# Optimization experiments

Measured on AMD Instinct MI355X. Metric: run time of the kernel, lower is better.

## Reference

```python
import jax, jax.numpy as jnp
import numpy as np

N, FR, P, B = 8192, 128, 4194304, 64
LH1, LH2 = 128, 64

def _mlp(x, W1, b1, W2, b2, W3, b3):
    h = jnp.tanh(x @ W1 + b1)
    h = jnp.tanh(h @ W2 + b2)
    return h @ W3 + b3  # [N, 1]

def setup_inputs() -> dict:
    key = jax.random.key(0)
    ks = jax.random.split(key, 12)
    r = jax.random.normal(ks[0], (N, FR), jnp.float32)
    xyz = jax.random.uniform(ks[1], (N, 3), jnp.float32) * 60.0  # box so distances >> sigma
    p0 = jax.random.randint(ks[2], (P,), 0, N)
    off = jax.random.randint(ks[3], (P,), 1, N)  # avoid self-pairs (D2=0)
    pairs = jnp.stack([p0, (p0 + off) % N], axis=1).astype(jnp.int32)
    num_pairs = jnp.full((B,), P // B, dtype=jnp.int32)
    def lin(k, fin, fout):
        return (jax.random.normal(k, (fin, fout), jnp.float32) / np.sqrt(fin)).astype(jnp.float32)
    sW1, sW2, sW3 = lin(ks[4], FR, LH1), lin(ks[5], LH1, LH2), lin(ks[6], LH2, 1)
    eW1, eW2, eW3 = lin(ks[7], FR, LH1), lin(ks[8], LH1, LH2), lin(ks[9], LH2, 1)
    z1, z2, z3 = jnp.zeros((LH1,), jnp.float32), jnp.zeros((LH2,), jnp.float32), jnp.zeros((1,), jnp.float32)
    return dict(r=r, xyz=xyz, pairs=pairs, num_pairs=num_pairs,
                sW1=sW1, sb1=z1, sW2=sW2, sb2=z2, sW3=sW3, sb3=z3,
                eW1=eW1, eb1=z1, eW2=eW2, eb2=z2, eW3=eW3, eb3=z3)

def reference(r, xyz, pairs, num_pairs, sW1, sb1, sW2, sb2, sW3, sb3,
              eW1, eb1, eW2, eb2, eW3, eb3):
    # D2 gathered at pairs == squared distance between the two atoms of each pair
    dx = xyz[pairs[:, 1]] - xyz[pairs[:, 0]]          # [P, 3]
    D2 = jnp.sum(dx * dx, axis=1, keepdims=True)       # [P, 1]
    inv_D = D2 ** -0.5
    sigma = 4.0 + 10.0 * _mlp(r, sW1, sb1, sW2, sb2, sW3, sb3) ** 2   # [N, 1]
    epsilon = 0.1 * _mlp(r, eW1, eb1, eW2, eb2, eW3, eb3) ** 2        # [N, 1]
    sigma_mixed = jnp.sqrt(sigma[pairs[:, 0]] * sigma[pairs[:, 1]])    # [P, 1]
    epsilon_mixed = jnp.sqrt(epsilon[pairs[:, 0]] * epsilon[pairs[:, 1]])
    s = sigma_mixed * inv_D
    s6 = s ** 6
    E_pair = 4.0 * epsilon_mixed * (s6 * s6 - s6)       # [P, 1]
    seg = jnp.repeat(jnp.arange(B), num_pairs, total_repeat_length=P)
    E = jax.ops.segment_sum(E_pair, seg, num_segments=B)  # [B, 1]
    return E
```

## Files before the change

### kernel.cpp

```cpp
#include <hip/hip_runtime.h>
#include <hip/hip_fp16.h>

#define NATOM 8192
#define FR    128
#define NSEG  64
#define NPROD 128
#define NBLK  256
#define PT    1024
#define PPT   16
#define SENT  0x5EED1234

typedef _Float16 v8h __attribute__((ext_vector_type(8)));
typedef _Float16 v4h __attribute__((ext_vector_type(4)));
typedef float    v4f __attribute__((ext_vector_type(4)));

__device__ __forceinline__ float fast_tanh(float x)
{
    float t = __expf(2.f * x);
    return 1.f - 2.f * __builtin_amdgcn_rcpf(t + 1.f);
}

__device__ __forceinline__ float pair_e(const float4* atomd, int ia, int ib)
{
    float4 A = atomd[ia], B = atomd[ib];
    float dx = A.x - B.x, dy = A.y - B.y, dz = A.z - B.z;
    float D2 = fmaf(dx, dx, fmaf(dy, dy, dz * dz));
    float inv = __builtin_amdgcn_rcpf(D2);
    float inv3 = inv * inv * inv;
    __half2 ha = __builtin_bit_cast(__half2, A.w);
    __half2 hb = __builtin_bit_cast(__half2, B.w);
    float pp = __low2float(ha) * __low2float(hb);
    float qq = __high2float(ha) * __high2float(hb);
    float s6 = pp * pp * inv3;
    return 4.f * qq * (s6 * s6 - s6);
}

__global__ __launch_bounds__(PT, 4) void k_fused(
    const float* __restrict__ r, const float* __restrict__ xyz,
    const int* __restrict__ pairs, const int* __restrict__ num_pairs,
    const float* __restrict__ w1s, const float* __restrict__ b1s,
    const float* __restrict__ w2s, const float* __restrict__ b2s,
    const float* __restrict__ w3s, const float* __restrict__ b3s,
    const float* __restrict__ w1e, const float* __restrict__ b1e,
    const float* __restrict__ w2e, const float* __restrict__ b2e,
    const float* __restrict__ w3e, const float* __restrict__ b3e,
    float4* __restrict__ atomd, int* __restrict__ flags,
    float* __restrict__ out, int P)
{
    extern __shared__ char ldsraw[];
    const int tid = threadIdx.x;
    const int bid = blockIdx.x;
    const bool prod = (bid < NPROD);

    if (bid == 0 && tid < NSEG) out[tid] = 0.f;

    const int base = (bid * PT + tid) * PPT;
    const bool fast = (base + PPT <= P);
    int pr2[PPT * 2];

    if ((!prod || tid >= 512) && fast) {
        const int4* pp4 = (const int4*)(pairs + (size_t)base * 2);
#pragma unroll
        for (int i = 0; i < PPT / 2; ++i) {
            int4 v = pp4[i];
            pr2[4*i] = v.x; pr2[4*i+1] = v.y; pr2[4*i+2] = v.z; pr2[4*i+3] = v.w;
        }
    }

    {
        _Float16* Wh  = (_Float16*)ldsraw;
        _Float16* Wl  = Wh + 32768;
        _Float16* h1h = Wh;
        _Float16* h1l = Wh + 16384;
        _Float16* W2h = Wh + 32768;
        _Float16* W2l = Wh + 49152;
        float*    mArr = (float*)(ldsraw + 131072);

        const int a0  = bid * 64;
        const int l = tid & 63, wv = tid >> 6;
        const int row16 = l & 15, kgrp = l >> 4;
        const int at = wv & 3, chf = wv >> 2;
        const bool mlp = prod && (tid < 512);

        v8h rh[4], rl[4];
        if (mlp) {
#pragma unroll
            for (int i = 0; i < 8; ++i) {
                int g = i * 512 + tid;
                int c = g & 255, ch = g >> 8;
                const float* wp = (c < 128) ? (w1s + c) : (w1e + (c - 128));
                v8h hh, ll;
#pragma unroll
                for (int j = 0; j < 8; ++j) {
                    float x = wp[(ch * 8 + j) * 128];
                    _Float16 h = (_Float16)x;
                    hh[j] = h;
                    ll[j] = (_Float16)((x - (float)h) * 4096.f);
                }
                int sw = c * 16 + (ch ^ (c & 15));
                *(v8h*)(Wh + sw * 8) = hh;
                *(v8h*)(Wl + sw * 8) = ll;
            }
            const float* rb = r + (size_t)(a0 + at * 16 + row16) * FR + kgrp * 8;
#pragma unroll
            for (int ks = 0; ks < 4; ++ks) {
                float4 x0 = *(const float4*)(rb + ks * 32);
                float4 x1 = *(const float4*)(rb + ks * 32 + 4);
                float xs[8] = {x0.x, x0.y, x0.z, x0.w, x1.x, x1.y, x1.z, x1.w};
#pragma unroll
                for (int j = 0; j < 8; ++j) {
                    _Float16 h = (_Float16)xs[j];
                    rh[ks][j] = h;
                    rl[ks][j] = (_Float16)((xs[j] - (float)h) * 4096.f);
                }
            }
        }
        __syncthreads();

        v4h hpack[8], lpack[8];
        if (mlp) {
#pragma unroll
            for (int ct = 0; ct < 8; ++ct) {
                int crow = chf * 128 + ct * 16 + row16;
                v4f a = {0.f, 0.f, 0.f, 0.f}, cr = {0.f, 0.f, 0.f, 0.f};
                int rbo = crow * 128, sw = crow & 15;
#pragma unroll
                for (int ks = 0; ks < 4; ++ks) {
                    int off = rbo + (((ks * 4 + kgrp) ^ sw) * 8);
                    v8h wh = *(const v8h*)(Wh + off);
                    v8h wl = *(const v8h*)(Wl + off);
                    a  = __builtin_amdgcn_mfma_f32_16x16x32_f16(wh, rh[ks], a,  0, 0, 0);
                    cr = __builtin_amdgcn_mfma_f32_16x16x32_f16(wh, rl[ks], cr, 0, 0, 0);
                    cr = __builtin_amdgcn_mfma_f32_16x16x32_f16(wl, rh[ks], cr, 0, 0, 0);
                }
                int colb = chf * 128 + ct * 16 + kgrp * 4;
                const float* bp = (colb < 128) ? (b1s + colb) : (b1e + (colb - 128));
                float4 bv = *(const float4*)bp;
                float bvx[4] = {bv.x, bv.y, bv.z, bv.w};
#pragma unroll
                for (int j = 0; j < 4; ++j) {
                    float v = fast_tanh(a[j] + cr[j] * 2.44140625e-4f + bvx[j]);
                    _Float16 h = (_Float16)v;
                    hpack[ct][j] = h;
                    lpack[ct][j] = (_Float16)((v - (float)h) * 4096.f);
                }
            }
        }
        __syncthreads();

        if (mlp) {
            int arow = at * 16 + row16;
#pragma unroll
            for (int ct = 0; ct < 8; ++ct) {
                int colb = chf * 128 + ct * 16 + kgrp * 4;
                int chs = (colb >> 3) ^ row16;
                int off = arow * 256 + chs * 8 + (colb & 7);
                *(v4h*)(h1h + off) = hpack[ct];
                *(v4h*)(h1l + off) = lpack[ct];
            }
#pragma unroll
            for (int i = 0; i < 4; ++i) {
                int g = i * 512 + tid;
                int c = g & 127, ch = g >> 7;
                const float* wp = (c < 64) ? (w2s + c) : (w2e + (c - 64));
                v8h hh, ll;
#pragma unroll
                for (int j = 0; j < 8; ++j) {
                    float x = wp[(ch * 8 + j) * 64];
                    _Float16 h = (_Float16)x;
                    hh[j] = h;
                    ll[j] = (_Float16)((x - (float)h) * 4096.f);
                }
                int sw = c * 16 + (ch ^ (c & 15));
                *(v8h*)(W2h + sw * 8) = hh;
                *(v8h*)(W2l + sw * 8) = ll;
            }
        }
        __syncthreads();

        if (mlp) {
            const int arow = at * 16 + row16;
            v8h bh[4], bl[4];
#pragma unroll
            for (int ks = 0; ks < 4; ++ks) {
                int chunk = chf * 16 + ks * 4 + kgrp;
                int off = arow * 256 + ((chunk ^ row16) * 8);
                bh[ks] = *(const v8h*)(h1h + off);
                bl[ks] = *(const v8h*)(h1l + off);
            }
            float ps = 0.f;
#pragma unroll
            for (int ct2 = 0; ct2 < 4; ++ct2) {
                int c2 = chf * 64 + ct2 * 16 + row16;
                v4f a = {0.f, 0.f, 0.f, 0.f}, cr = {0.f, 0.f, 0.f, 0.f};
                int rbo = c2 * 128, sw = c2 & 15;
#pragma unroll
                for (int ks = 0; ks < 4; ++ks) {
                    int off = rbo + (((ks * 4 + kgrp) ^ sw) * 8);
                    v8h wh = *(const v8h*)(W2h + off);
                    v8h wl = *(const v8h*)(W2l + off);
                    a  = __builtin_amdgcn_mfma_f32_16x16x32_f16(wh, bh[ks], a,  0, 0, 0);
                    cr = __builtin_amdgcn_mfma_f32_16x16x32_f16(wh, bl[ks], cr, 0, 0, 0);
                    cr = __builtin_amdgcn_mfma_f32_16x16x32_f16(wl, bh[ks], cr, 0, 0, 0);
                }
                int cb = ct2 * 16 + kgrp * 4;
                float4 b2v = *(const float4*)((chf ? b2e : b2s) + cb);
                float4 w3v = *(const float4*)((chf ? w3e : w3s) + cb);
                float b2x[4] = {b2v.x, b2v.y, b2v.z, b2v.w};
                float w3x[4] = {w3v.x, w3v.y, w3v.z, w3v.w};
#pragma unroll
                for (int j = 0; j < 4; ++j) {
                    float h2 = fast_tanh(a[j] + cr[j] * 2.44140625e-4f + b2x[j]);
                    ps = fmaf(h2, w3x[j], ps);
                }
            }
            ps += __shfl_xor(ps, 16);
            ps += __shfl_xor(ps, 32);
            if (l < 16) mArr[chf * 64 + at * 16 + l] = ps + (chf ? b3e[0] : b3s[0]);
        }
        __syncthreads();

        if (prod && tid < 64) {
            int atom = a0 + tid;
            float ms = mArr[tid], me = mArr[64 + tid];
            float sg = fmaf(10.f * ms, ms, 4.f);
            float p  = sg * sqrtf(sg);
            float q  = 0.31622776601683794f * fabsf(me);
            __half2 pq = __halves2half2(__float2half(p), __float2half(q));
            atomd[atom] = make_float4(xyz[3 * atom], xyz[3 * atom + 1],
                                      xyz[3 * atom + 2], __builtin_bit_cast(float, pq));
        }
        __syncthreads();
        if (prod && tid == 0) {
            __threadfence();
            __hip_atomic_store(&flags[bid], SENT, __ATOMIC_RELEASE, __HIP_MEMORY_SCOPE_AGENT);
        }
    }

    if (prod && tid < 512 && fast) {
        const int4* pp4 = (const int4*)(pairs + (size_t)base * 2);
#pragma unroll
        for (int i = 0; i < PPT / 2; ++i) {
            int4 v = pp4[i];
            pr2[4*i] = v.x; pr2[4*i+1] = v.y; pr2[4*i+2] = v.z; pr2[4*i+3] = v.w;
        }
    }

    if (tid < NPROD) {
        while (__hip_atomic_load(&flags[tid], __ATOMIC_ACQUIRE, __HIP_MEMORY_SCOPE_AGENT) != SENT)
            __builtin_amdgcn_s_sleep(8);
    }
    __syncthreads();

    {
        float4* atomdL = (float4*)ldsraw;
        int*    off    = (int*)(ldsraw + 131072);
        float*  bsum   = (float*)(ldsraw + 131072 + 272);

#pragma unroll
        for (int i = 0; i < NATOM / PT; ++i) atomdL[i * PT + tid] = atomd[i * PT + tid];
        if (tid < 64) {
            int run = num_pairs[tid];
#pragma unroll
            for (int d = 1; d < 64; d <<= 1) {
                int o = __shfl_up(run, d);
                if (tid >= d) run += o;
            }
            off[tid + 1] = run;
            if (tid == 0) off[0] = 0;
            bsum[tid] = 0.f;
        }
        __syncthreads();

        if (__all(fast)) {
            int s = 0;
#pragma unroll
            for (int st = 32; st; st >>= 1) { int ns = s + st; if (ns <= NSEG - 1 && off[ns] <= base) s = ns; }
            float acc = 0.f;
            if (base + PPT <= off[s + 1] || s == NSEG - 1) {
#pragma unroll
                for (int i = 0; i < PPT; ++i)
                    acc += pair_e(atomdL, pr2[2 * i], pr2[2 * i + 1]);
            } else {
                int off_next = off[s + 1];
#pragma unroll
                for (int i = 0; i < PPT; ++i) {
                    int idx = base + i;
                    while (s < NSEG - 1 && idx >= off_next) {
                        if (acc != 0.f) atomicAdd(&bsum[s], acc);
                        acc = 0.f; ++s; off_next = off[s + 1];
                    }
                    acc += pair_e(atomdL, pr2[2 * i], pr2[2 * i + 1]);
                }
            }
            int s0 = __builtin_amdgcn_readfirstlane(s);
            if (__all(s == s0)) {
                float v = acc;
#pragma unroll
                for (int o = 32; o; o >>= 1) v += __shfl_xor(v, o);
                if ((tid & 63) == 0) atomicAdd(&bsum[s0], v);
            } else {
                atomicAdd(&bsum[s], acc);
            }
        } else if (base < P) {
            int s = 0;
#pragma unroll
            for (int st = 32; st; st >>= 1) { int ns = s + st; if (ns <= NSEG - 1 && off[ns] <= base) s = ns; }
            int off_next = off[s + 1];
            float acc = 0.f;
            for (int i = 0; i < PPT; ++i) {
                int idx = base + i;
                if (idx >= P) break;
                while (s < NSEG - 1 && idx >= off_next) {
                    if (acc != 0.f) atomicAdd(&bsum[s], acc);
                    acc = 0.f; ++s; off_next = off[s + 1];
                }
                acc += pair_e(atomdL, pairs[2 * (size_t)idx], pairs[2 * (size_t)idx + 1]);
            }
            if (acc != 0.f) atomicAdd(&bsum[s], acc);
        }
        __syncthreads();
        if (tid < NSEG) atomicAdd(&out[tid], bsum[tid]);
    }
}

extern "C" void kernel_launch(void* const* d_in, const int* in_sizes, int n_in,
                              void* d_out, int out_size, void* d_ws, size_t ws_size,
                              hipStream_t stream)
{
    const float* r    = (const float*)d_in[0];
    const float* xyz  = (const float*)d_in[1];
    const int*   prs  = (const int*)d_in[2];
    const int*   np   = (const int*)d_in[3];
    const float* sW1  = (const float*)d_in[4];
    const float* sb1  = (const float*)d_in[5];
    const float* sW2  = (const float*)d_in[6];
    const float* sb2  = (const float*)d_in[7];
    const float* sW3  = (const float*)d_in[8];
    const float* sb3  = (const float*)d_in[9];
    const float* eW1  = (const float*)d_in[10];
    const float* eb1  = (const float*)d_in[11];
    const float* eW2  = (const float*)d_in[12];
    const float* eb2  = (const float*)d_in[13];
    const float* eW3  = (const float*)d_in[14];
    const float* eb3  = (const float*)d_in[15];
    float* out = (float*)d_out;
    const int P = in_sizes[2] / 2;

    float4* atomd = (float4*)d_ws;
    int*    flags = (int*)((char*)d_ws + 131072);

    size_t smem = 131072 + 272 + 256;
    hipFuncSetAttribute((const void*)k_fused, hipFuncAttributeMaxDynamicSharedMemorySize, (int)smem);
    k_fused<<<NBLK, PT, smem, stream>>>(r, xyz, prs, np,
                                        sW1, sb1, sW2, sb2, sW3, sb3,
                                        eW1, eb1, eW2, eb2, eW3, eb3,
                                        atomd, flags, out, P);
}
```

Measured before the change: 40.22 us.

## Spread MLP over all blocks with 512-thread blocks and 32 pairs per thread

Every one of the 256 blocks now computes the MLP for 32 atoms using all of its 512 threads, instead of 128 producer blocks of 1024 threads where half the threads sat idle. The second layer is split into halves, and the partial outputs are summed when the per-atom data is built. Each thread now handles 32 pairs, prefetched after the MLP phase, and every block waits on 256 flags instead of 128. In exchange, all 256 blocks must stage W1 and W2 into LDS, which repeats that load work, and more registers are used per thread for pair indices.

After: 46.92 us. 1.17x slower.

```diff
diff --git a/kernel.cpp b/kernel.cpp
--- a/kernel.cpp
+++ b/kernel.cpp
@@ -4,10 +4,9 @@
 #define NATOM 8192
 #define FR    128
 #define NSEG  64
-#define NPROD 128
 #define NBLK  256
-#define PT    1024
-#define PPT   16
+#define PT    512
+#define PPT   32
 #define SENT  0x5EED1234
 
 typedef _Float16 v8h __attribute__((ext_vector_type(8)));
@@ -35,7 +34,7 @@
     return 4.f * qq * (s6 * s6 - s6);
 }
 
-__global__ __launch_bounds__(PT, 4) void k_fused(
+__global__ __launch_bounds__(PT) void k_fused(
     const float* __restrict__ r, const float* __restrict__ xyz,
     const int* __restrict__ pairs, const int* __restrict__ num_pairs,
     const float* __restrict__ w1s, const float* __restrict__ b1s,
@@ -50,57 +49,43 @@
     extern __shared__ char ldsraw[];
     const int tid = threadIdx.x;
     const int bid = blockIdx.x;
-    const bool prod = (bid < NPROD);
 
     if (bid == 0 && tid < NSEG) out[tid] = 0.f;
-
-    const int base = (bid * PT + tid) * PPT;
-    const bool fast = (base + PPT <= P);
-    int pr2[PPT * 2];
-
-    if ((!prod || tid >= 512) && fast) {
-        const int4* pp4 = (const int4*)(pairs + (size_t)base * 2);
-#pragma unroll
-        for (int i = 0; i < PPT / 2; ++i) {
-            int4 v = pp4[i];
-            pr2[4*i] = v.x; pr2[4*i+1] = v.y; pr2[4*i+2] = v.z; pr2[4*i+3] = v.w;
-        }
-    }
 
     {
         _Float16* Wh  = (_Float16*)ldsraw;
         _Float16* Wl  = Wh + 32768;
         _Float16* h1h = Wh;
-        _Float16* h1l = Wh + 16384;
-        _Float16* W2h = Wh + 32768;
-        _Float16* W2l = Wh + 49152;
+        _Float16* h1l = Wh + 8192;
+        _Float16* W2h = Wh + 16384;
+        _Float16* W2l = Wh + 32768;
         float*    mArr = (float*)(ldsraw + 131072);
 
-        const int a0  = bid * 64;
+        const int a0  = bid * 32;
         const int l = tid & 63, wv = tid >> 6;
         const int row16 = l & 15, kgrp = l >> 4;
-        const int at = wv & 3, chf = wv >> 2;
-        const bool mlp = prod && (tid < 512);
+        const int at = wv & 1, cq = wv >> 1;
+
+#pragma unroll
+        for (int i = 0; i < 8; ++i) {
+            int g = i * 512 + tid;
+            int c = g & 255, ch = g >> 8;
+            const float* wp = (c < 128) ? (w1s + c) : (w1e + (c - 128));
+            v8h hh, ll;
+#pragma unroll
+            for (int j = 0; j < 8; ++j) {
+                float x = wp[(ch * 8 + j) * 128];
+                _Float16 h = (_Float16)x;
+                hh[j] = h;
+                ll[j] = (_Float16)((x - (float)h) * 4096.f);
+            }
+            int sw = c * 16 + (ch ^ (c & 15));
+            *(v8h*)(Wh + sw * 8) = hh;
+            *(v8h*)(Wl + sw * 8) = ll;
+        }
 
         v8h rh[4], rl[4];
-        if (mlp) {
-#pragma unroll
-            for (int i = 0; i < 8; ++i) {
-                int g = i * 512 + tid;
-                int c = g & 255, ch = g >> 8;
-                const float* wp = (c < 128) ? (w1s + c) : (w1e + (c - 128));
-                v8h hh, ll;
-#pragma unroll
-                for (int j = 0; j < 8; ++j) {
-                    float x = wp[(ch * 8 + j) * 128];
-                    _Float16 h = (_Float16)x;
-                    hh[j] = h;
-                    ll[j] = (_Float16)((x - (float)h) * 4096.f);
-                }
-                int sw = c * 16 + (ch ^ (c & 15));
-                *(v8h*)(Wh + sw * 8) = hh;
-                *(v8h*)(Wl + sw * 8) = ll;
-            }
+        {
             const float* rb = r + (size_t)(a0 + at * 16 + row16) * FR + kgrp * 8;
 #pragma unroll
             for (int ks = 0; ks < 4; ++ks) {
@@ -117,42 +102,40 @@
         }
         __syncthreads();
 
-        v4h hpack[8], lpack[8];
-        if (mlp) {
-#pragma unroll
-            for (int ct = 0; ct < 8; ++ct) {
-                int crow = chf * 128 + ct * 16 + row16;
-                v4f a = {0.f, 0.f, 0.f, 0.f}, cr = {0.f, 0.f, 0.f, 0.f};
-                int rbo = crow * 128, sw = crow & 15;
-#pragma unroll
-                for (int ks = 0; ks < 4; ++ks) {
-                    int off = rbo + (((ks * 4 + kgrp) ^ sw) * 8);
-                    v8h wh = *(const v8h*)(Wh + off);
-                    v8h wl = *(const v8h*)(Wl + off);
-                    a  = __builtin_amdgcn_mfma_f32_16x16x32_f16(wh, rh[ks], a,  0, 0, 0);
-                    cr = __builtin_amdgcn_mfma_f32_16x16x32_f16(wh, rl[ks], cr, 0, 0, 0);
-                    cr = __builtin_amdgcn_mfma_f32_16x16x32_f16(wl, rh[ks], cr, 0, 0, 0);
-                }
-                int colb = chf * 128 + ct * 16 + kgrp * 4;
-                const float* bp = (colb < 128) ? (b1s + colb) : (b1e + (colb - 128));
-                float4 bv = *(const float4*)bp;
-                float bvx[4] = {bv.x, bv.y, bv.z, bv.w};
-#pragma unroll
-                for (int j = 0; j < 4; ++j) {
-                    float v = fast_tanh(a[j] + cr[j] * 2.44140625e-4f + bvx[j]);
-                    _Float16 h = (_Float16)v;
-                    hpack[ct][j] = h;
-                    lpack[ct][j] = (_Float16)((v - (float)h) * 4096.f);
-                }
-            }
-        }
-        __syncthreads();
-
-        if (mlp) {
+        v4h hpack[4], lpack[4];
+#pragma unroll
+        for (int ct = 0; ct < 4; ++ct) {
+            int crow = cq * 64 + ct * 16 + row16;
+            v4f a = {0.f, 0.f, 0.f, 0.f}, cr = {0.f, 0.f, 0.f, 0.f};
+            int rbo = crow * 128, sw = crow & 15;
+#pragma unroll
+            for (int ks = 0; ks < 4; ++ks) {
+                int off = rbo + (((ks * 4 + kgrp) ^ sw) * 8);
+                v8h wh = *(const v8h*)(Wh + off);
+                v8h wl = *(const v8h*)(Wl + off);
+                a  = __builtin_amdgcn_mfma_f32_16x16x32_f16(wh, rh[ks], a,  0, 0, 0);
+                cr = __builtin_amdgcn_mfma_f32_16x16x32_f16(wh, rl[ks], cr, 0, 0, 0);
+                cr = __builtin_amdgcn_mfma_f32_16x16x32_f16(wl, rh[ks], cr, 0, 0, 0);
+            }
+            int colb = cq * 64 + ct * 16 + kgrp * 4;
+            const float* bp = (colb < 128) ? (b1s + colb) : (b1e + (colb - 128));
+            float4 bv = *(const float4*)bp;
+            float bvx[4] = {bv.x, bv.y, bv.z, bv.w};
+#pragma unroll
+            for (int j = 0; j < 4; ++j) {
+                float v = fast_tanh(a[j] + cr[j] * 2.44140625e-4f + bvx[j]);
+                _Float16 h = (_Float16)v;
+                hpack[ct][j] = h;
+                lpack[ct][j] = (_Float16)((v - (float)h) * 4096.f);
+            }
+        }
+        __syncthreads();
+
+        {
             int arow = at * 16 + row16;
 #pragma unroll
-            for (int ct = 0; ct < 8; ++ct) {
-                int colb = chf * 128 + ct * 16 + kgrp * 4;
+            for (int ct = 0; ct < 4; ++ct) {
+                int colb = cq * 64 + ct * 16 + kgrp * 4;
                 int chs = (colb >> 3) ^ row16;
                 int off = arow * 256 + chs * 8 + (colb & 7);
                 *(v4h*)(h1h + off) = hpack[ct];
@@ -178,20 +161,21 @@
         }
         __syncthreads();
 
-        if (mlp) {
+        {
+            const int path = cq >> 1, half = cq & 1;
             const int arow = at * 16 + row16;
             v8h bh[4], bl[4];
 #pragma unroll
             for (int ks = 0; ks < 4; ++ks) {
-                int chunk = chf * 16 + ks * 4 + kgrp;
+                int chunk = path * 16 + ks * 4 + kgrp;
                 int off = arow * 256 + ((chunk ^ row16) * 8);
                 bh[ks] = *(const v8h*)(h1h + off);
                 bl[ks] = *(const v8h*)(h1l + off);
             }
             float ps = 0.f;
 #pragma unroll
-            for (int ct2 = 0; ct2 < 4; ++ct2) {
-                int c2 = chf * 64 + ct2 * 16 + row16;
+            for (int ct2 = 0; ct2 < 2; ++ct2) {
+                int c2 = path * 64 + half * 32 + ct2 * 16 + row16;
                 v4f a = {0.f, 0.f, 0.f, 0.f}, cr = {0.f, 0.f, 0.f, 0.f};
                 int rbo = c2 * 128, sw = c2 & 15;
 #pragma unroll
@@ -203,9 +187,9 @@
                     cr = __builtin_amdgcn_mfma_f32_16x16x32_f16(wh, bl[ks], cr, 0, 0, 0);
                     cr = __builtin_amdgcn_mfma_f32_16x16x32_f16(wl, bh[ks], cr, 0, 0, 0);
                 }
-                int cb = ct2 * 16 + kgrp * 4;
-                float4 b2v = *(const float4*)((chf ? b2e : b2s) + cb);
-                float4 w3v = *(const float4*)((chf ? w3e : w3s) + cb);
+                int cb = half * 32 + ct2 * 16 + kgrp * 4;
+                float4 b2v = *(const float4*)((path ? b2e : b2s) + cb);
+                float4 w3v = *(const float4*)((path ? w3e : w3s) + cb);
                 float b2x[4] = {b2v.x, b2v.y, b2v.z, b2v.w};
                 float w3x[4] = {w3v.x, w3v.y, w3v.z, w3v.w};
 #pragma unroll
@@ -216,13 +200,14 @@
             }
             ps += __shfl_xor(ps, 16);
             ps += __shfl_xor(ps, 32);
-            if (l < 16) mArr[chf * 64 + at * 16 + l] = ps + (chf ? b3e[0] : b3s[0]);
-        }
-        __syncthreads();
-
-        if (prod && tid < 64) {
+            if (l < 16) mArr[cq * 32 + at * 16 + l] = ps;
+        }
+        __syncthreads();
+
+        if (tid < 32) {
             int atom = a0 + tid;
-            float ms = mArr[tid], me = mArr[64 + tid];
+            float ms = mArr[tid] + mArr[32 + tid] + b3s[0];
+            float me = mArr[64 + tid] + mArr[96 + tid] + b3e[0];
             float sg = fmaf(10.f * ms, ms, 4.f);
             float p  = sg * sqrtf(sg);
             float q  = 0.31622776601683794f * fabsf(me);
@@ -231,13 +216,16 @@
                                       xyz[3 * atom + 2], __builtin_bit_cast(float, pq));
         }
         __syncthreads();
-        if (prod && tid == 0) {
+        if (tid == 0) {
             __threadfence();
             __hip_atomic_store(&flags[bid], SENT, __ATOMIC_RELEASE, __HIP_MEMORY_SCOPE_AGENT);
         }
     }
 
-    if (prod && tid < 512 && fast) {
+    const int base = (bid * PT + tid) * PPT;
+    const bool fast = (base + PPT <= P);
+    int pr2[PPT * 2];
+    if (fast) {
         const int4* pp4 = (const int4*)(pairs + (size_t)base * 2);
 #pragma unroll
         for (int i = 0; i < PPT / 2; ++i) {
@@ -246,7 +234,7 @@
         }
     }
 
-    if (tid < NPROD) {
+    if (tid < NBLK) {
         while (__hip_atomic_load(&flags[tid], __ATOMIC_ACQUIRE, __HIP_MEMORY_SCOPE_AGENT) != SENT)
             __builtin_amdgcn_s_sleep(8);
     }
```
